# Performance work log

Measured on AMD Instinct MI355X. Metric: run time of the kernel, lower is better.

The kernel has to match this reference:

```python
import jax, jax.numpy as jnp
import numpy as np
from jax import lax

GEN_POLY = ("1111001", "1011011")  # rate 1/2, constraint length 7 (octal 171/133)


def build_trellis(gen_poly):
    """Feed-forward (non-recursive) convolutional trellis tables.

    State = shift-register contents, most-recent bit is the MSB of the state
    index. Returns int32 tables, each [ns, ni]:
      to_nodes[s, b]        : next state from state s with input bit b
      op_by_fromnode[s, b]  : emitted output-symbol index for (s, b)
      from_nodes[j, m]      : m-th predecessor state of state j
      ip_by_tonode[j, m]    : input bit taken on that predecessor transition
    """
    mu = len(gen_poly[0]) - 1
    ns, ni = 2 ** mu, 2
    g = np.array([[int(c) for c in p] for p in gen_poly])  # [conv_n, mu+1]
    to_nodes = np.zeros((ns, ni), np.int32)
    op_by_fromnode = np.zeros((ns, ni), np.int32)
    from_nodes = np.zeros((ns, ni), np.int32)
    ip_by_tonode = np.zeros((ns, ni), np.int32)
    fill = np.zeros(ns, np.int32)
    for s in range(ns):
        rbits = [(s >> (mu - 1 - j)) & 1 for j in range(mu)]
        for b in range(ni):
            w = np.array([b] + rbits)                 # full window [b, r0..r_{mu-1}]
            obits = (g @ w) % 2                        # output bits, MSB first
            o = int("".join(str(int(x)) for x in obits), 2)
            j = int("".join(str(x) for x in ([b] + rbits[:-1])), 2)
            to_nodes[s, b] = j
            op_by_fromnode[s, b] = o
            from_nodes[j, fill[j]] = s
            ip_by_tonode[j, fill[j]] = b
            fill[j] += 1
    return to_nodes, op_by_fromnode, from_nodes, ip_by_tonode


TO_NODES, OP_BY_FROM, FROM_NODES, IP_BY_TO = build_trellis(GEN_POLY)
CONV_N = len(GEN_POLY)
MU = len(GEN_POLY[0]) - 1
NS = 2 ** MU
NO = 2 ** CONV_N
# output-symbol bit patterns, MSB first, mapped to signs (1-2*bit)
_OP_BITS = np.array([[(o >> (CONV_N - 1 - j)) & 1 for j in range(CONV_N)]
                     for o in range(NO)], np.float32)
OP_SIGN = jnp.asarray(1.0 - 2.0 * _OP_BITS)  # [NO, CONV_N]
IP_SIGN = jnp.asarray([1.0, -1.0])           # sign of input bit b: 1-2b


def setup_inputs() -> dict:
    key = jax.random.key(0)
    k1, k2 = jax.random.split(key)
    B, n = 256, 4096
    T = n // CONV_N  # = k = 2048 info bits
    llr_ch = jax.random.normal(k1, (B, n), dtype=jnp.float32)
    llr_a = jax.random.normal(k2, (B, T), dtype=jnp.float32)
    return {"llr_ch": llr_ch, "llr_a": llr_a}


def _bcjr(llr_ch, llr_a):
    B, n = llr_ch.shape
    T = n // CONV_N
    # branch metrics: bm[t, b, o] = exp(0.5 * sum_j llr[b, t, j] * (1-2*opbit_j(o)))
    llr_r = llr_ch.reshape(B, T, CONV_N)
    bm = jnp.exp(0.5 * jnp.einsum('btj,oj->tbo', llr_r, OP_SIGN))  # [T, B, NO]
    llr_a_t = llr_a.T  # [T, B]

    def gamma_fn(bm_t, la_t):
        # a-priori factor exp(0.5*llr_a*(1-2b)) times channel branch metric
        ap = jnp.exp(0.5 * la_t[:, None, None] * IP_SIGN[None, None, :])  # [B,1,2]
        return ap * bm_t[:, OP_BY_FROM]  # [B, NS, 2]

    alpha0 = jnp.zeros((B, NS), jnp.float32).at[:, 0].set(1.0)

    def fwd(alpha_prev, inp):
        bm_t, la_t = inp
        gam = gamma_fn(bm_t, la_t)                        # [B, NS, 2] by from-state
        ag = gam * alpha_prev[:, :, None]                  # alpha_{t} * gamma_t
        agt = ag[:, FROM_NODES, IP_BY_TO]                  # regroup by to-state
        alpha = agt.sum(-1)
        alpha = alpha / alpha.sum(-1, keepdims=True)       # normalize (as in TF code)
        return alpha, alpha_prev                            # emit alpha BEFORE step t

    _, alphas = lax.scan(fwd, alpha0, (bm, llr_a_t))       # alphas[t] = alpha_t, [T,B,NS]

    beta_T = jnp.full((B, NS), 1.0 / NS, jnp.float32)      # non-terminated: uniform

    def bwd(beta_next, inp):
        bm_t, la_t, alpha_t = inp
        gam = gamma_fn(bm_t, la_t)                         # [B, NS, 2]
        bg = gam * beta_next[:, TO_NODES]                  # gamma * beta_{t+1}(to)
        beta = bg.sum(-1)
        beta = beta / beta.sum(-1, keepdims=True)
        joint = alpha_t[:, :, None] * bg                   # APP per (state, bit)
        llr_t = jnp.log(joint[..., 0].sum(-1)) - jnp.log(joint[..., 1].sum(-1))
        return beta, llr_t

    _, llrs_rev = lax.scan(bwd, beta_T, (bm[::-1], llr_a_t[::-1], alphas[::-1]))
    return llrs_rev[::-1].T  # [B, T] soft LLRs (hard_out=False)


def reference(llr_ch, llr_a):
    return _bcjr(llr_ch, llr_a)
```

## Files before the change

### kernel.cpp

```cpp
#include <hip/hip_runtime.h>

#define T_LEN 2048
#define NSTATE 64
#define NCHUNK 16
#define CH_S 128
#define WARM 64
#define RK 16

template <int CTRL>
__device__ __forceinline__ float dpp_add(float v) {
    int r = __builtin_amdgcn_update_dpp(0, __float_as_int(v), CTRL, 0xF, 0xF, true);
    return v + __int_as_float(r);
}
__device__ __forceinline__ float red63(float v) {
    v = dpp_add<0x111>(v);
    v = dpp_add<0x112>(v);
    v = dpp_add<0x114>(v);
    v = dpp_add<0x118>(v);
    v = dpp_add<0x142>(v);
    v = dpp_add<0x143>(v);
    return v;
}
__device__ __forceinline__ float bcast63(float v) {
    return __uint_as_float(__builtin_amdgcn_readlane(__float_as_uint(v), 63));
}
__device__ __forceinline__ float pair_sum_xor1(float v) {
    return dpp_add<0xB1>(v);
}
__device__ __forceinline__ unsigned short bf16_of(float f) {
    return (unsigned short)((__float_as_uint(f) + 0x8000u) >> 16);
}
__device__ __forceinline__ float bf16_lo(unsigned u) { return __uint_as_float(u << 16); }
__device__ __forceinline__ float bf16_hi(unsigned u) { return __uint_as_float(u & 0xffff0000u); }


__global__ __launch_bounds__(256, 4)
void bcjr_beta_kernel(const float* __restrict__ llr_ch,
                      const float* __restrict__ llr_a,
                      unsigned short* __restrict__ wsB)
{
    const int wave  = blockIdx.x * 4 + (threadIdx.x >> 6);
    const int lane  = threadIdx.x & 63;
    const int chunk = wave & (NCHUNK - 1);
    const int b     = wave >> 4;

    const float c0 = 1.0f - 2.0f * (float)(__popc(lane & 57) & 1);
    const float c1 = 1.0f - 2.0f * (float)(__popc(lane & 27) & 1);
    const float kE = 0.5f * 1.442695040888963f;
    const float k0 = kE * c0, k1 = kE * c1;

    const float* chp = llr_ch + (size_t)b * (2 * T_LEN);
    const float* lap = llr_a  + (size_t)b * T_LEN;
    unsigned short* w = wsB + (size_t)b * T_LEN * NSTATE;

    const int bs0 = lane >> 1;
    const int bs1 = 32 + (lane >> 1);
    const int t0 = chunk * CH_S;
    const int te = (chunk == NCHUNK - 1) ? (t0 + CH_S) : (t0 + CH_S + WARM);
    float state = 1.0f / 64.0f;

    for (int g = te - RK; g >= t0; g -= RK) {
        const bool store = (g < t0 + CH_S);
        #pragma unroll
        for (int h = 1; h >= 0; --h) {
            const int gb = g + 8 * h;
            const float4* c4 = (const float4*)(chp + 2 * gb);
            const float4* a4 = (const float4*)(lap + gb);
            float4 cc[4], aa[2];
            #pragma unroll
            for (int i = 0; i < 4; ++i) cc[i] = c4[i];
            #pragma unroll
            for (int i = 0; i < 2; ++i) aa[i] = a4[i];
            unsigned short* wb = w + (size_t)gb * NSTATE + lane;
            #pragma unroll
            for (int i = 7; i >= 0; --i) {
                float l0 = (i & 1) ? cc[i >> 1].z : cc[i >> 1].x;
                float l1 = (i & 1) ? cc[i >> 1].w : cc[i >> 1].y;
                float la = ((const float*)aa)[i];
                if (store) wb[i * NSTATE] = bf16_of(state);
                float x   = fmaf(la, kE, fmaf(l0, k0, l1 * k1));
                float g0v = exp2f(x);
                float g1v = __builtin_amdgcn_rcpf(g0v);
                float t0v = __shfl(state, bs0, 64);
                float t1v = __shfl(state, bs1, 64);
                state = fmaf(g0v, t0v, g1v * t1v);
            }
        }
        float s = bcast63(red63(state));
        state = state * __builtin_amdgcn_rcpf(s);
    }
}

__global__ __launch_bounds__(256, 4)
void bcjr_alpha_llr_kernel(const float* __restrict__ llr_ch,
                           const float* __restrict__ llr_a,
                           const unsigned short* __restrict__ wsB,
                           float* __restrict__ out)
{
    const int wave  = blockIdx.x * 4 + (threadIdx.x >> 6);
    const int lane  = threadIdx.x & 63;
    const int chunk = wave & (NCHUNK - 1);
    const int b     = wave >> 4;

    const float c0 = 1.0f - 2.0f * (float)(__popc(lane & 57) & 1);
    const float c1 = 1.0f - 2.0f * (float)(__popc(lane & 27) & 1);
    const float kE = 0.5f * 1.442695040888963f;
    const float k0 = kE * c0, k1 = kE * c1;
    const float LN2 = 0.69314718055994531f;

    const float* chp = llr_ch + (size_t)b * (2 * T_LEN);
    const float* lap = llr_a  + (size_t)b * T_LEN;
    float* outp      = out    + (size_t)b * T_LEN;

    const int  fs0 = 2 * (lane & 31);
    const bool fhi = (lane >= 32);
    const int t0 = chunk * CH_S;
    const int ts = (chunk == 0) ? t0 : t0 - WARM;
    float state = (chunk == 0) ? ((lane == 0) ? 1.0f : 0.0f) : (1.0f / 64.0f);

    for (int g = ts; g < t0; g += RK) {
        #pragma unroll
        for (int h = 0; h < 2; ++h) {
            const int gb = g + 8 * h;
            const float4* c4 = (const float4*)(chp + 2 * gb);
            const float4* a4 = (const float4*)(lap + gb);
            float4 cc[4], aa[2];
            #pragma unroll
            for (int i = 0; i < 4; ++i) cc[i] = c4[i];
            #pragma unroll
            for (int i = 0; i < 2; ++i) aa[i] = a4[i];
            #pragma unroll
            for (int i = 0; i < 8; ++i) {
                float l0 = (i & 1) ? cc[i >> 1].z : cc[i >> 1].x;
                float l1 = (i & 1) ? cc[i >> 1].w : cc[i >> 1].y;
                float la = ((const float*)aa)[i];
                float x   = fmaf(la, kE, fmaf(l0, k0, l1 * k1));
                float g0v = exp2f(x);
                float g1v = __builtin_amdgcn_rcpf(g0v);
                float s0  = pair_sum_xor1(state * g0v);
                float s1  = pair_sum_xor1(state * g1v);
                float a0  = __shfl(s0, fs0, 64);
                float a1  = __shfl(s1, fs0, 64);
                state = fhi ? a1 : a0;
            }
        }
        float s = bcast63(red63(state));
        state = state * __builtin_amdgcn_rcpf(s);
    }

    const unsigned* brow = (const unsigned*)(wsB + (size_t)b * T_LEN * NSTATE);
    const int  di0 = lane >> 2;
    const int  di1 = 16 + (lane >> 2);
    const bool dhi = (lane & 2) != 0;
    float keep = 0.0f;

    for (int g = t0; g < t0 + CH_S; g += RK) {
        #pragma unroll
        for (int h = 0; h < 2; ++h) {
            const int gb = g + 8 * h;
            const float4* c4 = (const float4*)(chp + 2 * gb);
            const float4* a4 = (const float4*)(lap + gb);
            float4 cc[4], aa[2];
            #pragma unroll
            for (int i = 0; i < 4; ++i) cc[i] = c4[i];
            #pragma unroll
            for (int i = 0; i < 2; ++i) aa[i] = a4[i];
            unsigned bu0[8], bu1[8];
            const unsigned* r = brow + (size_t)gb * 32;
            #pragma unroll
            for (int i = 0; i < 8; ++i) { bu0[i] = r[i * 32 + di0]; bu1[i] = r[i * 32 + di1]; }
            #pragma unroll
            for (int i = 0; i < 8; ++i) {
                const int t = gb + i;
                float l0 = (i & 1) ? cc[i >> 1].z : cc[i >> 1].x;
                float l1 = (i & 1) ? cc[i >> 1].w : cc[i >> 1].y;
                float la = ((const float*)aa)[i];
                float x   = fmaf(la, kE, fmaf(l0, k0, l1 * k1));
                float g0v = exp2f(x);
                float g1v = __builtin_amdgcn_rcpf(g0v);
                float b0v = dhi ? bf16_hi(bu0[i]) : bf16_lo(bu0[i]);
                float b1v = dhi ? bf16_hi(bu1[i]) : bf16_lo(bu1[i]);
                float ag0 = state * g0v;
                float ag1 = state * g1v;
                float n0 = red63(ag0 * b0v);
                float n1 = red63(ag1 * b1v);
                float llr = LN2 * (__log2f(n0) - __log2f(n1));
                float lb  = bcast63(llr);
                keep = (lane == (t & 63)) ? lb : keep;
                float s0 = pair_sum_xor1(ag0);
                float s1 = pair_sum_xor1(ag1);
                float a0 = __shfl(s0, fs0, 64);
                float a1 = __shfl(s1, fs0, 64);
                state = fhi ? a1 : a0;
            }
        }
        if ((g & 63) == 48) outp[g - 48 + lane] = keep;
        float s = bcast63(red63(state));
        state = state * __builtin_amdgcn_rcpf(s);
    }
}

extern "C" void kernel_launch(void* const* d_in, const int* in_sizes, int n_in,
                              void* d_out, int out_size, void* d_ws, size_t ws_size,
                              hipStream_t stream) {
    const float* llr_ch = (const float*)d_in[0];
    const float* llr_a  = (const float*)d_in[1];
    float* out = (float*)d_out;
    unsigned short* wsB = (unsigned short*)d_ws;

    int B = in_sizes[0] / (2 * T_LEN);
    int n_waves = B * NCHUNK;
    hipLaunchKernelGGL(bcjr_beta_kernel, dim3(n_waves / 4), dim3(256), 0, stream,
                       llr_ch, llr_a, wsB);
    hipLaunchKernelGGL(bcjr_alpha_llr_kernel, dim3(n_waves / 4), dim3(256), 0, stream,
                       llr_ch, llr_a, wsB, out);
}
```

Before: 151.7 us.

## Split beta into more chunks and compute LLR from updated alpha with half-wave reductions

The beta kernel now splits each frame into 32 chunks of 64 steps instead of 16 of 128, which doubles the number of waves and raises the occupancy hint to 8. This shortens the serial backward recursion per wave, at the cost of more warm-up work in total. In the alpha/LLR kernel, the LLR now uses the already-updated alpha (indexed by to-state) times beta of the next state. The two numerator sums come from one half-wave DPP reduction read at lanes 31 and 63, replacing two full reductions, two beta loads per step and a broadcast. This removes redundant reductions and loads from the serial critical path.

Measured after the change: 142.2 us. 6.2% less time.

```diff
diff --git a/kernel.cpp b/kernel.cpp
--- a/kernel.cpp
+++ b/kernel.cpp
@@ -5,6 +5,8 @@
 #define NCHUNK 16
 #define CH_S 128
 #define WARM 64
+#define NCH_B 32
+#define CH_B 64
 #define RK 16
 
 template <int CTRL>
@@ -21,12 +23,19 @@
     v = dpp_add<0x143>(v);
     return v;
 }
-__device__ __forceinline__ float bcast63(float v) {
-    return __uint_as_float(__builtin_amdgcn_readlane(__float_as_uint(v), 63));
-}
-__device__ __forceinline__ float pair_sum_xor1(float v) {
-    return dpp_add<0xB1>(v);
-}
+__device__ __forceinline__ float red_half(float v) {
+    v = dpp_add<0x111>(v);
+    v = dpp_add<0x112>(v);
+    v = dpp_add<0x114>(v);
+    v = dpp_add<0x118>(v);
+    v = dpp_add<0x142>(v);
+    return v;
+}
+__device__ __forceinline__ float rdlane(float v, int l) {
+    return __uint_as_float(__builtin_amdgcn_readlane(__float_as_uint(v), l));
+}
+__device__ __forceinline__ float bcast63(float v) { return rdlane(v, 63); }
+__device__ __forceinline__ float pair_sum_xor1(float v) { return dpp_add<0xB1>(v); }
 __device__ __forceinline__ unsigned short bf16_of(float f) {
     return (unsigned short)((__float_as_uint(f) + 0x8000u) >> 16);
 }
@@ -34,15 +43,15 @@
 __device__ __forceinline__ float bf16_hi(unsigned u) { return __uint_as_float(u & 0xffff0000u); }
 
 
-__global__ __launch_bounds__(256, 4)
+__global__ __launch_bounds__(256, 8)
 void bcjr_beta_kernel(const float* __restrict__ llr_ch,
                       const float* __restrict__ llr_a,
                       unsigned short* __restrict__ wsB)
 {
     const int wave  = blockIdx.x * 4 + (threadIdx.x >> 6);
     const int lane  = threadIdx.x & 63;
-    const int chunk = wave & (NCHUNK - 1);
-    const int b     = wave >> 4;
+    const int chunk = wave & (NCH_B - 1);
+    const int b     = wave >> 5;
 
     const float c0 = 1.0f - 2.0f * (float)(__popc(lane & 57) & 1);
     const float c1 = 1.0f - 2.0f * (float)(__popc(lane & 27) & 1);
@@ -55,12 +64,12 @@
 
     const int bs0 = lane >> 1;
     const int bs1 = 32 + (lane >> 1);
-    const int t0 = chunk * CH_S;
-    const int te = (chunk == NCHUNK - 1) ? (t0 + CH_S) : (t0 + CH_S + WARM);
+    const int t0 = chunk * CH_B;
+    const int te = (chunk == NCH_B - 1) ? (t0 + CH_B) : (t0 + CH_B + WARM);
     float state = 1.0f / 64.0f;
 
     for (int g = te - RK; g >= t0; g -= RK) {
-        const bool store = (g < t0 + CH_S);
+        const bool store = (g < t0 + CH_B);
         #pragma unroll
         for (int h = 1; h >= 0; --h) {
             const int gb = g + 8 * h;
@@ -149,9 +158,8 @@
     }
 
     const unsigned* brow = (const unsigned*)(wsB + (size_t)b * T_LEN * NSTATE);
-    const int  di0 = lane >> 2;
-    const int  di1 = 16 + (lane >> 2);
-    const bool dhi = (lane & 2) != 0;
+    const int  bdw = lane >> 1;
+    const bool bhi = (lane & 1) != 0;
     float keep = 0.0f;
 
     for (int g = t0; g < t0 + CH_S; g += RK) {
@@ -165,10 +173,10 @@
             for (int i = 0; i < 4; ++i) cc[i] = c4[i];
             #pragma unroll
             for (int i = 0; i < 2; ++i) aa[i] = a4[i];
-            unsigned bu0[8], bu1[8];
+            unsigned bu[8];
             const unsigned* r = brow + (size_t)gb * 32;
             #pragma unroll
-            for (int i = 0; i < 8; ++i) { bu0[i] = r[i * 32 + di0]; bu1[i] = r[i * 32 + di1]; }
+            for (int i = 0; i < 8; ++i) bu[i] = r[i * 32 + bdw];
             #pragma unroll
             for (int i = 0; i < 8; ++i) {
                 const int t = gb + i;
@@ -178,20 +186,20 @@
                 float x   = fmaf(la, kE, fmaf(l0, k0, l1 * k1));
                 float g0v = exp2f(x);
                 float g1v = __builtin_amdgcn_rcpf(g0v);
-                float b0v = dhi ? bf16_hi(bu0[i]) : bf16_lo(bu0[i]);
-                float b1v = dhi ? bf16_hi(bu1[i]) : bf16_lo(bu1[i]);
                 float ag0 = state * g0v;
                 float ag1 = state * g1v;
-                float n0 = red63(ag0 * b0v);
-                float n1 = red63(ag1 * b1v);
+                float s0  = pair_sum_xor1(ag0);
+                float s1  = pair_sum_xor1(ag1);
+                float a0  = __shfl(s0, fs0, 64);
+                float a1  = __shfl(s1, fs0, 64);
+                float an  = fhi ? a1 : a0;
+                float bv  = bhi ? bf16_hi(bu[i]) : bf16_lo(bu[i]);
+                float v   = red_half(an * bv);
+                float n0  = rdlane(v, 31);
+                float n1  = rdlane(v, 63);
                 float llr = LN2 * (__log2f(n0) - __log2f(n1));
-                float lb  = bcast63(llr);
-                keep = (lane == (t & 63)) ? lb : keep;
-                float s0 = pair_sum_xor1(ag0);
-                float s1 = pair_sum_xor1(ag1);
-                float a0 = __shfl(s0, fs0, 64);
-                float a1 = __shfl(s1, fs0, 64);
-                state = fhi ? a1 : a0;
+                keep = (lane == (t & 63)) ? llr : keep;
+                state = an;
             }
         }
         if ((g & 63) == 48) outp[g - 48 + lane] = keep;
@@ -209,9 +217,10 @@
     unsigned short* wsB = (unsigned short*)d_ws;
 
     int B = in_sizes[0] / (2 * T_LEN);
-    int n_waves = B * NCHUNK;
-    hipLaunchKernelGGL(bcjr_beta_kernel, dim3(n_waves / 4), dim3(256), 0, stream,
+    int nw_beta  = B * NCH_B;
+    int nw_alpha = B * NCHUNK;
+    hipLaunchKernelGGL(bcjr_beta_kernel, dim3(nw_beta / 4), dim3(256), 0, stream,
                        llr_ch, llr_a, wsB);
-    hipLaunchKernelGGL(bcjr_alpha_llr_kernel, dim3(n_waves / 4), dim3(256), 0, stream,
+    hipLaunchKernelGGL(bcjr_alpha_llr_kernel, dim3(nw_alpha / 4), dim3(256), 0, stream,
                        llr_ch, llr_a, wsB, out);
 }
```
